# Optimization experiments

Hardware: AMD Instinct MI355X
Metric: run time of the kernel (lower is better)

The kernel has to match this reference:

```python
import jax, jax.numpy as jnp
import numpy as np
from jax import lax

LEAK = 0.2
EPS = 1e-5
T = 20  # sequence_length


def _lrelu(x):
    return jnp.where(x >= 0, x, LEAK * x)


def _deconv(x, w, stride=2, k=4, p=1):
    # PyTorch ConvTranspose2d(weight [in,out,kH,kW], stride=2, pad=1) equivalent:
    # flip kernel spatially, swap in/out channels, use lhs_dilation.
    wt = jnp.flip(w, (2, 3)).transpose(1, 0, 2, 3)  # OIHW
    pad = k - 1 - p
    return lax.conv_general_dilated(
        x, wt, window_strides=(1, 1), padding=[(pad, pad), (pad, pad)],
        lhs_dilation=(stride, stride),
        dimension_numbers=('NCHW', 'OIHW', 'NCHW'))


def _bn(x, g, b):
    # BatchNorm2d, training mode (batch statistics, biased variance)
    m = x.mean((0, 2, 3), keepdims=True)
    v = x.var((0, 2, 3), keepdims=True)
    return (x - m) * lax.rsqrt(v + EPS) * g[None, :, None, None] + b[None, :, None, None]


def setup_inputs() -> dict:
    B, CD, MD, H, FF = 64, 128, 128, 256, 512
    ks = jax.random.split(jax.random.key(0), 32)
    rn = lambda k, sh, s=0.02: (s * jax.random.normal(k, sh)).astype(jnp.float32)
    return {
        'z_content': jax.random.normal(ks[0], (B, CD), jnp.float32),
        'z_motion': jax.random.normal(ks[1], (B, MD), jnp.float32),
        'W_h': rn(ks[2], (H, CD + MD)), 'b_h': jnp.zeros((H,), jnp.float32),
        'W_c': rn(ks[3], (H, CD + MD)), 'b_c': jnp.zeros((H,), jnp.float32),
        'W_ih': rn(ks[4], (4 * H, H)), 'W_hh': rn(ks[5], (4 * H, H)),
        'b_ih': jnp.zeros((4 * H,), jnp.float32), 'b_hh': jnp.zeros((4 * H,), jnp.float32),
        'W_f': rn(ks[6], (FF, H)), 'b_f': jnp.zeros((FF,), jnp.float32),
        'init_in': rn(ks[7], (1, H), 0.1),
        'fc_W': rn(ks[8], (256 * 4 * 4, FF + CD)), 'fc_b': jnp.zeros((256 * 16,), jnp.float32),
        'w0': rn(ks[9], (256, 128, 4, 4)), 'g0': jnp.ones((128,), jnp.float32), 'be0': jnp.zeros((128,), jnp.float32),
        'w1': rn(ks[10], (128, 64, 4, 4)), 'g1': jnp.ones((64,), jnp.float32), 'be1': jnp.zeros((64,), jnp.float32),
        'w2': rn(ks[11], (64, 32, 4, 4)), 'g2': jnp.ones((32,), jnp.float32), 'be2': jnp.zeros((32,), jnp.float32),
        'wf': rn(ks[12], (32, 1, 4, 4)), 'bf': jnp.zeros((1,), jnp.float32),
    }


def reference(z_content, z_motion, W_h, b_h, W_c, b_c, W_ih, W_hh, b_ih, b_hh,
              W_f, b_f, init_in, fc_W, fc_b, w0, g0, be0, w1, g1, be1,
              w2, g2, be2, wf, bf):
    B = z_content.shape[0]
    z = jnp.concatenate([z_content, z_motion], axis=-1)
    h0 = z @ W_h.T + b_h  # [B,H]
    c0 = z @ W_c.T + b_c
    x0 = jnp.broadcast_to(init_in, (B, init_in.shape[1]))
    bias = b_ih + b_hh

    def step(carry, _):
        x, h, c = carry
        gates = x @ W_ih.T + h @ W_hh.T + bias  # [B,4H], torch gate order i,f,g,o
        i, f, g, o = jnp.split(gates, 4, axis=-1)
        c_new = jax.nn.sigmoid(f) * c + jax.nn.sigmoid(i) * jnp.tanh(g)
        h_new = jax.nn.sigmoid(o) * jnp.tanh(c_new)
        return (h_new, h_new, c_new), h_new

    _, outs = lax.scan(step, (x0, h0, c0), None, length=T)  # [T,B,H]
    outs = outs.transpose(1, 0, 2)  # [B,T,H]

    ff = _lrelu(outs @ W_f.T + b_f)  # [B,T,FF]
    zc = jnp.broadcast_to(z_content[:, None, :], (B, T, z_content.shape[1]))
    feat = jnp.concatenate([ff, zc], axis=-1).reshape(B * T, -1)  # [B*T, FF+CD]

    h = _lrelu(feat @ fc_W.T + fc_b).reshape(B * T, 256, 4, 4)
    h = _lrelu(_bn(_deconv(h, w0), g0, be0))   # [B*T,128,8,8]
    h = _lrelu(_bn(_deconv(h, w1), g1, be1))   # [B*T,64,16,16]
    h = _lrelu(_bn(_deconv(h, w2), g2, be2))   # [B*T,32,32,32]
    out = jax.nn.sigmoid(_deconv(h, wf) + bf[None, :, None, None])  # [B*T,1,64,64]
    return out.reshape(B, T, *out.shape[1:])
```

## Files before the change

kernel.cpp:

```cpp
#include <hip/hip_runtime.h>
#include <hip/hip_bf16.h>
#include <math.h>

typedef __hip_bfloat16 bf16;
typedef __attribute__((ext_vector_type(8))) short bf16x8;
typedef __attribute__((ext_vector_type(4))) float f32x4;
typedef __attribute__((ext_vector_type(2))) float f32x2;

#define LRELU(v) ((v) > 0.f ? (v) : 0.2f*(v))

__device__ __forceinline__ float sig_f(float x){ return 1.f/(1.f + __expf(-x)); }
__device__ __forceinline__ float tanh_f(float x){
  float ax = fabsf(x);
  float e = __expf(-2.f*ax);
  float t = (1.f - e)/(1.f + e);
  return x >= 0.f ? t : -t;
}
__device__ __forceinline__ ushort bfbits(float v){
  bf16 b = __float2bfloat16(v);
  return *(ushort*)&b;
}
__device__ __forceinline__ uint bfpack(float a, float b){
  return (uint)bfbits(a) | ((uint)bfbits(b) << 16);
}
__device__ __forceinline__ float bflo(uint u){ return __uint_as_float(u << 16); }
__device__ __forceinline__ float bfhi(uint u){ return __uint_as_float(u & 0xffff0000u); }

__global__ void k_tobf16(const float* __restrict__ src, ushort* __restrict__ dst, int n){
  int i = blockIdx.x*256 + threadIdx.x;
  if (i < n) dst[i] = bfbits(src[i]);
}

__global__ void k_transpose(const float* __restrict__ src, float* __restrict__ dst, int R, int C){
  __shared__ float t[32][33];
  int c0 = blockIdx.x*32, r0 = blockIdx.y*32;
  int tx = threadIdx.x, ty = threadIdx.y;
  #pragma unroll
  for (int i = 0; i < 4; ++i)
    t[ty+8*i][tx] = src[(size_t)(r0+ty+8*i)*C + c0+tx];
  __syncthreads();
  #pragma unroll
  for (int i = 0; i < 4; ++i)
    dst[(size_t)(c0+ty+8*i)*R + r0+tx] = t[tx][ty+8*i];
}

__global__ void k_w4prep(const float* __restrict__ Wih, const float* __restrict__ Whh,
                         uint4* __restrict__ Whq8, uint4* __restrict__ Wsq8,
                         float* __restrict__ stats){
  int k4 = blockIdx.x, j = threadIdx.x;
  if (k4 < 2) { int i = k4*256 + j; if (i < 448) stats[i] = 0.f; }
  uint h4[4], s4[4];
  #pragma unroll
  for (int d = 0; d < 4; ++d) {
    int k = 4*k4 + d;
    float hi = Whh[j*256+k],       hf = Whh[(256+j)*256+k];
    float hg = Whh[(512+j)*256+k], ho = Whh[(768+j)*256+k];
    float ii = Wih[j*256+k],       iff = Wih[(256+j)*256+k];
    float ig = Wih[(512+j)*256+k], io = Wih[(768+j)*256+k];
    int lo = __builtin_amdgcn_cvt_pk_fp8_f32(hi, hf, 0, false);
    h4[d] = (uint)__builtin_amdgcn_cvt_pk_fp8_f32(hg, ho, lo, true);
    lo = __builtin_amdgcn_cvt_pk_fp8_f32(hi+ii, hf+iff, 0, false);
    s4[d] = (uint)__builtin_amdgcn_cvt_pk_fp8_f32(hg+ig, ho+io, lo, true);
  }
  Whq8[k4*256+j] = make_uint4(h4[0], h4[1], h4[2], h4[3]);
  Wsq8[k4*256+j] = make_uint4(s4[0], s4[1], s4[2], s4[3]);
}

__global__ void k_xgbias(const float* __restrict__ Wih, const float* __restrict__ b_ih,
                         const float* __restrict__ b_hh, const float* __restrict__ init_in,
                         float4* __restrict__ xg4, float4* __restrict__ bias4){
  int b = blockIdx.x, t = threadIdx.x;
  float v = init_in[t];
  float p0 = v * Wih[b*256 + t];
  float p1 = v * Wih[(256+b)*256 + t];
  float p2 = v * Wih[(512+b)*256 + t];
  float p3 = v * Wih[(768+b)*256 + t];
  #pragma unroll
  for (int o = 32; o; o >>= 1) {
    p0 += __shfl_xor(p0, o); p1 += __shfl_xor(p1, o);
    p2 += __shfl_xor(p2, o); p3 += __shfl_xor(p3, o);
  }
  __shared__ float4 red[4];
  int lane = t & 63, wid = t >> 6;
  if (lane == 0) red[wid] = make_float4(p0,p1,p2,p3);
  __syncthreads();
  if (t == 0) {
    float4 bi = make_float4(b_ih[b]+b_hh[b], b_ih[256+b]+b_hh[256+b],
                            b_ih[512+b]+b_hh[512+b], b_ih[768+b]+b_hh[768+b]);
    bias4[b] = bi;
    float4 a = bi;
    #pragma unroll
    for (int w = 0; w < 4; ++w) { a.x += red[w].x; a.y += red[w].y; a.z += red[w].z; a.w += red[w].w; }
    xg4[b] = a;
  }
}

__global__ __launch_bounds__(256) void k_h0c0(const float* __restrict__ zc, const float* __restrict__ zm,
                      const float* __restrict__ WhT, const float* __restrict__ WcT,
                      const float* __restrict__ b_h, const float* __restrict__ b_c,
                      float* __restrict__ h, float* __restrict__ c){
  __shared__ float zs[256];
  int b = blockIdx.x, j = threadIdx.x;
  zs[j] = (j < 128) ? zc[b*128 + j] : zm[b*128 + (j-128)];
  __syncthreads();
  float ah = b_h[j], ac = b_c[j];
  #pragma unroll 4
  for (int k = 0; k < 256; ++k) {
    float zv = zs[k];
    ah = fmaf(zv, WhT[k*256 + j], ah);
    ac = fmaf(zv, WcT[k*256 + j], ac);
  }
  h[b*256+j] = ah; c[b*256+j] = ac;
}

__global__ __launch_bounds__(1024) void k_lstm_all(
    const uint4* __restrict__ Whq8, const uint4* __restrict__ Wsq8,
    const float4* __restrict__ xg4, const float4* __restrict__ bias4,
    const float* __restrict__ h0, const float* __restrict__ c0,
    ushort* __restrict__ outsb){
  __shared__ float hs[256];
  __shared__ float4 part[3][256];
  const int b = blockIdx.x, tid = threadIdx.x;
  const int j = tid & 255, kq = tid >> 8;
  float cj = 0.f;
  if (kq == 0) { hs[j] = h0[b*256 + j]; cj = c0[b*256 + j]; }
  __syncthreads();
  for (int t = 0; t < 20; ++t) {
    const uint4* __restrict__ Wp = ((t == 0) ? Whq8 : Wsq8) + (size_t)(kq*16)*256 + j;
    float4 a = make_float4(0.f, 0.f, 0.f, 0.f);
    #pragma unroll 8
    for (int kk = 0; kk < 16; ++kk) {
      uint4 wv = Wp[(size_t)kk*256];
      const float* __restrict__ hb = &hs[kq*64 + 4*kk];
      {
        f32x2 pif = __builtin_amdgcn_cvt_pk_f32_fp8((int)wv.x, false);
        f32x2 pgo = __builtin_amdgcn_cvt_pk_f32_fp8((int)wv.x, true);
        float hv = hb[0];
        a.x = fmaf(hv, pif[0], a.x); a.y = fmaf(hv, pif[1], a.y);
        a.z = fmaf(hv, pgo[0], a.z); a.w = fmaf(hv, pgo[1], a.w);
      }
      {
        f32x2 pif = __builtin_amdgcn_cvt_pk_f32_fp8((int)wv.y, false);
        f32x2 pgo = __builtin_amdgcn_cvt_pk_f32_fp8((int)wv.y, true);
        float hv = hb[1];
        a.x = fmaf(hv, pif[0], a.x); a.y = fmaf(hv, pif[1], a.y);
        a.z = fmaf(hv, pgo[0], a.z); a.w = fmaf(hv, pgo[1], a.w);
      }
      {
        f32x2 pif = __builtin_amdgcn_cvt_pk_f32_fp8((int)wv.z, false);
        f32x2 pgo = __builtin_amdgcn_cvt_pk_f32_fp8((int)wv.z, true);
        float hv = hb[2];
        a.x = fmaf(hv, pif[0], a.x); a.y = fmaf(hv, pif[1], a.y);
        a.z = fmaf(hv, pgo[0], a.z); a.w = fmaf(hv, pgo[1], a.w);
      }
      {
        f32x2 pif = __builtin_amdgcn_cvt_pk_f32_fp8((int)wv.w, false);
        f32x2 pgo = __builtin_amdgcn_cvt_pk_f32_fp8((int)wv.w, true);
        float hv = hb[3];
        a.x = fmaf(hv, pif[0], a.x); a.y = fmaf(hv, pif[1], a.y);
        a.z = fmaf(hv, pgo[0], a.z); a.w = fmaf(hv, pgo[1], a.w);
      }
    }
    if (kq) part[kq-1][j] = a;
    __syncthreads();
    if (kq == 0) {
      float4 p1 = part[0][j], p2 = part[1][j], p3 = part[2][j];
      float4 bb = (t == 0) ? xg4[j] : bias4[j];
      a.x += p1.x + p2.x + p3.x + bb.x;
      a.y += p1.y + p2.y + p3.y + bb.y;
      a.z += p1.z + p2.z + p3.z + bb.z;
      a.w += p1.w + p2.w + p3.w + bb.w;
      float ig = sig_f(a.x), fg = sig_f(a.y), gg = tanh_f(a.z), og = sig_f(a.w);
      cj = fmaf(fg, cj, ig*gg);
      float hj = og * tanh_f(cj);
      outsb[(b*20 + t)*256 + j] = bfbits(hj);
      hs[j] = hj;
    }
    __syncthreads();
  }
}

__global__ void k_zc(const float* __restrict__ zc, ushort* __restrict__ featb){
  int e = blockIdx.x*256 + threadIdx.x;
  int r = e >> 7, c = e & 127;
  featb[r*640 + 512 + c] = bfbits(zc[(r/20)*128 + c]);
}

__global__ __launch_bounds__(256) void k_ff_m(
    const ushort* __restrict__ A, const ushort* __restrict__ W,
    const float* __restrict__ bias, ushort* __restrict__ C)
{
  constexpr int K = 256, BK = 64, NK = K/BK, BM = 128, BN = 64;
  constexpr int RS = 72;
  constexpr int NCF = BN/16;
  constexpr int AC = 4, WC = 2;

  __shared__ __align__(16) ushort Al[2][BM*RS];
  __shared__ __align__(16) ushort Wl[2][BN*RS];

  const int tid = threadIdx.x;
  const int col0 = blockIdx.x * BN, row0 = blockIdx.y * BM;
  const int w = tid >> 6, l = tid & 63, lm = l & 15, lk = l >> 4;

  f32x4 acc[NCF][2];
  #pragma unroll
  for (int m = 0; m < NCF; ++m)
    #pragma unroll
    for (int s = 0; s < 2; ++s)
      acc[m][s] = (f32x4){0.f,0.f,0.f,0.f};

  uint4 ar[AC], wr[WC];

  #define LOADG(kt) { \
    _Pragma("unroll") \
    for (int i = 0; i < AC; ++i) { \
      int chunk = tid + i*256; \
      int rl = chunk >> 3, kc = chunk & 7; \
      ar[i] = *(const uint4*)&A[(size_t)(row0+rl)*K + (kt)*BK + kc*8]; \
    } \
    _Pragma("unroll") \
    for (int i = 0; i < WC; ++i) { \
      int chunk = tid + i*256; \
      int co = chunk >> 3, kc = chunk & 7; \
      wr[i] = *(const uint4*)&W[(size_t)(col0+co)*K + (kt)*BK + kc*8]; \
    } }

  #define STOREL(buf) { \
    _Pragma("unroll") \
    for (int i = 0; i < AC; ++i) { \
      int chunk = tid + i*256; \
      int rl = chunk >> 3, kc = chunk & 7; \
      *(uint4*)&Al[buf][rl*RS + kc*8] = ar[i]; \
    } \
    _Pragma("unroll") \
    for (int i = 0; i < WC; ++i) { \
      int chunk = tid + i*256; \
      int co = chunk >> 3, kc = chunk & 7; \
      *(uint4*)&Wl[buf][co*RS + kc*8] = wr[i]; \
    } }

  LOADG(0);
  STOREL(0);
  int cur = 0;
  for (int kt = 0; kt < NK; ++kt) {
    if (kt + 1 < NK) LOADG(kt + 1);
    __syncthreads();
    #pragma unroll
    for (int kf = 0; kf < 2; ++kf) {
      bf16x8 bfr[2];
      #pragma unroll
      for (int s = 0; s < 2; ++s)
        bfr[s] = *(bf16x8*)&Al[cur][(w*32 + s*16 + lm)*RS + kf*32 + lk*8];
      #pragma unroll
      for (int m = 0; m < NCF; ++m) {
        bf16x8 afr = *(bf16x8*)&Wl[cur][(m*16 + lm)*RS + kf*32 + lk*8];
        acc[m][0] = __builtin_amdgcn_mfma_f32_16x16x32_bf16(afr, bfr[0], acc[m][0], 0, 0, 0);
        acc[m][1] = __builtin_amdgcn_mfma_f32_16x16x32_bf16(afr, bfr[1], acc[m][1], 0, 0, 0);
      }
    }
    if (kt + 1 < NK) STOREL(cur ^ 1);
    cur ^= 1;
  }

  #pragma unroll
  for (int m = 0; m < NCF; ++m) {
    #pragma unroll
    for (int s = 0; s < 2; ++s) {
      int row = row0 + w*32 + s*16 + lm;
      f32x4 v = acc[m][s];
      int u0 = col0 + m*16 + lk*4;
      union { ushort u[4]; uint2 q; } pk;
      #pragma unroll
      for (int j = 0; j < 4; ++j)
        pk.u[j] = bfbits(LRELU(v[j] + bias[u0+j]));
      *(uint2*)&C[(size_t)row*640 + u0] = pk.q;
    }
  }
  #undef LOADG
  #undef STOREL
}

__global__ __launch_bounds__(256) void k_gemm_fc_m(
    const ushort* __restrict__ A, const ushort* __restrict__ W,
    const float* __restrict__ bias, ushort* __restrict__ C)
{
  constexpr int K = 640, BK = 64, NK = K/BK, BM = 128, BN = 64;
  constexpr int RS = 72;
  constexpr int NCF = BN/16;
  constexpr int AC = 4, WC = 2;

  __shared__ __align__(16) ushort Al[2][BM*RS];
  __shared__ __align__(16) ushort Wl[2][BN*RS];

  const int tid = threadIdx.x;
  const int col0 = blockIdx.x * BN, row0 = blockIdx.y * BM;
  const int w = tid >> 6, l = tid & 63, lm = l & 15, lk = l >> 4;

  f32x4 acc[NCF][2];
  #pragma unroll
  for (int m = 0; m < NCF; ++m)
    #pragma unroll
    for (int s = 0; s < 2; ++s)
      acc[m][s] = (f32x4){0.f,0.f,0.f,0.f};

  uint4 ar[AC], wr[WC];

  #define LOADG(kt) { \
    _Pragma("unroll") \
    for (int i = 0; i < AC; ++i) { \
      int chunk = tid + i*256; \
      int rl = chunk >> 3, kc = chunk & 7; \
      ar[i] = *(const uint4*)&A[(size_t)(row0+rl)*K + (kt)*BK + kc*8]; \
    } \
    _Pragma("unroll") \
    for (int i = 0; i < WC; ++i) { \
      int chunk = tid + i*256; \
      int co = chunk >> 3, kc = chunk & 7; \
      wr[i] = *(const uint4*)&W[(size_t)(col0+co)*K + (kt)*BK + kc*8]; \
    } }

  #define STOREL(buf) { \
    _Pragma("unroll") \
    for (int i = 0; i < AC; ++i) { \
      int chunk = tid + i*256; \
      int rl = chunk >> 3, kc = chunk & 7; \
      *(uint4*)&Al[buf][rl*RS + kc*8] = ar[i]; \
    } \
    _Pragma("unroll") \
    for (int i = 0; i < WC; ++i) { \
      int chunk = tid + i*256; \
      int co = chunk >> 3, kc = chunk & 7; \
      *(uint4*)&Wl[buf][co*RS + kc*8] = wr[i]; \
    } }

  LOADG(0);
  STOREL(0);
  int cur = 0;
  for (int kt = 0; kt < NK; ++kt) {
    if (kt + 1 < NK) LOADG(kt + 1);
    __syncthreads();
    #pragma unroll
    for (int kf = 0; kf < 2; ++kf) {
      bf16x8 bfr[2];
      #pragma unroll
      for (int s = 0; s < 2; ++s)
        bfr[s] = *(bf16x8*)&Al[cur][(w*32 + s*16 + lm)*RS + kf*32 + lk*8];
      #pragma unroll
      for (int m = 0; m < NCF; ++m) {
        bf16x8 afr = *(bf16x8*)&Wl[cur][(m*16 + lm)*RS + kf*32 + lk*8];
        acc[m][0] = __builtin_amdgcn_mfma_f32_16x16x32_bf16(afr, bfr[0], acc[m][0], 0, 0, 0);
        acc[m][1] = __builtin_amdgcn_mfma_f32_16x16x32_bf16(afr, bfr[1], acc[m][1], 0, 0, 0);
      }
    }
    if (kt + 1 < NK) STOREL(cur ^ 1);
    cur ^= 1;
  }

  #pragma unroll
  for (int m = 0; m < NCF; ++m) {
    #pragma unroll
    for (int s = 0; s < 2; ++s) {
      int row = row0 + w*32 + s*16 + lm;
      f32x4 v = acc[m][s];
      #pragma unroll
      for (int j = 0; j < 4; ++j) {
        int u = col0 + m*16 + lk*4 + j;
        float val = LRELU(v[j] + bias[u]);
        C[((size_t)row << 12) + ((size_t)(u & 15) << 8) + (u >> 4)] = bfbits(val);
      }
    }
  }
  #undef LOADG
  #undef STOREL
}

template<int CI, int CO>
__global__ void k_wprep_im(const float* __restrict__ w, ushort* __restrict__ wpn){
  constexpr int K = 4*CI, KF = K/32, MMW2 = CO/16;
  int e = blockIdx.x*256 + threadIdx.x;
  if (e >= 16*CI*CO) return;
  int j  = e & 7;
  int lk = (e >> 3) & 3;
  int lm = (e >> 5) & 15;
  int r3 = e >> 9;
  int kf = r3 % KF; int r4 = r3 / KF;
  int m  = r4 % MMW2; int p = r4 / MMW2;
  int k  = kf*32 + lk*8 + j;
  int t  = k / CI, ci = k % CI;
  int co = m*16 + lm;
  int py = p >> 1, px = p & 1, dy = t >> 1, dx = t & 1;
  int ky = (py ? 0 : 1) + 2*dy;
  int kx = (px ? 0 : 1) + 2*dx;
  wpn[e] = bfbits(w[((ci*CO + co)*4 + ky)*4 + kx]);
}

__global__ void k_wfprep(const float* __restrict__ wf, ushort* __restrict__ wfb){
  int e = blockIdx.x*256 + threadIdx.x;
  if (e < 512) {
    int t = e >> 5, ci = e & 31;
    wfb[t*32 + ci] = bfbits(wf[ci*16 + t]);
  }
}

template<int CI, int CO, int HI>
__global__ __launch_bounds__(256) void k_dcv(
    const ushort* __restrict__ in, const ushort* __restrict__ wp,
    ushort* __restrict__ out, float* __restrict__ gsum, float* __restrict__ gsq)
{
  constexpr int WI = HI, HO = 2*HI, WO = 2*WI;
  constexpr int K = 4*CI, BK = 64, NK = K/BK, KFT = K/32;
  constexpr int BSP = 128;
  constexpr int RS = 72;
  constexpr int NCF = CO/16;
  constexpr int AC = BSP/32;

  __shared__ __align__(16) ushort Al[2][BSP*RS];
  __shared__ float s_sum[CO], s_sq[CO];

  const int tid = threadIdx.x;
  const int sp0 = blockIdx.x * BSP;
  const int p  = blockIdx.y;
  const int py = p >> 1, px = p & 1;
  const int w  = tid >> 6, l = tid & 63;
  const int lm = l & 15, lk = l >> 4;

  if (tid < CO) { s_sum[tid] = 0.f; s_sq[tid] = 0.f; }

  f32x4 acc[NCF][2];
  #pragma unroll
  for (int m = 0; m < NCF; ++m)
    #pragma unroll
    for (int s = 0; s < 2; ++s)
      acc[m][s] = (f32x4){0.f,0.f,0.f,0.f};

  uint4 ar[AC];
  const ushort* wpb = wp + (size_t)(p*NCF)*KFT*512;

  #define LOADT(kt) { \
    int t = ((kt)*BK)/CI, ci0 = ((kt)*BK)%CI; \
    int dy = t >> 1, dx = t & 1; \
    _Pragma("unroll") \
    for (int i = 0; i < AC; ++i) { \
      int chunk = tid + i*256; \
      int rl = chunk >> 3, kc = chunk & 7; \
      int r = sp0 + rl; \
      int n = r / (HI*WI), rem = r % (HI*WI); \
      int oy = rem / WI, ox = rem % WI; \
      int iy = oy + py - dy, ix = ox + px - dx; \
      if ((unsigned)iy < (unsigned)HI && (unsigned)ix < (unsigned)WI) \
        ar[i] = *(const uint4*)&in[((((size_t)n*HI + iy)*WI + ix)*CI) + ci0 + kc*8]; \
      else ar[i] = make_uint4(0,0,0,0); \
    } }

  #define STORET(buf) { \
    _Pragma("unroll") \
    for (int i = 0; i < AC; ++i) { \
      int chunk = tid + i*256; \
      int rl = chunk >> 3, kc = chunk & 7; \
      *(uint4*)&Al[buf][rl*RS + kc*8] = ar[i]; \
    } }

  LOADT(0);
  STORET(0);
  int cur = 0;
  for (int kt = 0; kt < NK; ++kt) {
    if (kt + 1 < NK) LOADT(kt + 1);
    __syncthreads();
    #pragma unroll
    for (int kf = 0; kf < 2; ++kf) {
      const int ktg = kt*2 + kf;
      bf16x8 bfr[2];
      #pragma unroll
      for (int s = 0; s < 2; ++s)
        bfr[s] = *(bf16x8*)&Al[cur][(w*32 + s*16 + lm)*RS + kf*32 + lk*8];
      #pragma unroll
      for (int m = 0; m < NCF; ++m) {
        bf16x8 afr = *(const bf16x8*)&wpb[((size_t)m*KFT + ktg)*512 + lm*32 + lk*8];
        acc[m][0] = __builtin_amdgcn_mfma_f32_16x16x32_bf16(afr, bfr[0], acc[m][0], 0, 0, 0);
        acc[m][1] = __builtin_amdgcn_mfma_f32_16x16x32_bf16(afr, bfr[1], acc[m][1], 0, 0, 0);
      }
    }
    if (kt + 1 < NK) STORET(cur ^ 1);
    cur ^= 1;
  }

  #pragma unroll
  for (int m = 0; m < NCF; ++m) {
    float s1[4] = {0,0,0,0}, s2[4] = {0,0,0,0};
    #pragma unroll
    for (int s = 0; s < 2; ++s) {
      f32x4 v = acc[m][s];
      #pragma unroll
      for (int j = 0; j < 4; ++j) { s1[j] += v[j]; s2[j] += v[j]*v[j]; }
    }
    #pragma unroll
    for (int j = 0; j < 4; ++j) {
      float a = s1[j], b = s2[j];
      #pragma unroll
      for (int o = 1; o < 16; o <<= 1) { a += __shfl_xor(a, o); b += __shfl_xor(b, o); }
      if (lm == 0) {
        atomicAdd(&s_sum[m*16 + lk*4 + j], a);
        atomicAdd(&s_sq [m*16 + lk*4 + j], b);
      }
    }
  }
  #pragma unroll
  for (int s = 0; s < 2; ++s) {
    int sp = sp0 + w*32 + s*16 + lm;
    int n = sp / (HI*WI), rem = sp % (HI*WI);
    int y = 2*(rem / WI) + py, x = 2*(rem % WI) + px;
    size_t ob = (((size_t)n*HO + y)*WO + x)*CO + lk*4;
    #pragma unroll
    for (int m = 0; m < NCF; ++m) {
      f32x4 v = acc[m][s];
      union { ushort u[4]; uint2 q; } pk;
      pk.u[0] = bfbits(v[0]); pk.u[1] = bfbits(v[1]);
      pk.u[2] = bfbits(v[2]); pk.u[3] = bfbits(v[3]);
      *(uint2*)&out[ob + m*16] = pk.q;
    }
  }
  __syncthreads();
  for (int cc = tid; cc < CO; cc += 256) {
    atomicAdd(&gsum[cc], s_sum[cc]);
    atomicAdd(&gsq[cc],  s_sq[cc]);
  }
  #undef LOADT
  #undef STORET
}

template<int CI, int CO, int HI>
__global__ __launch_bounds__(512) void k_dcvim(
    const ushort* __restrict__ in, const ushort* __restrict__ wp,
    const float* __restrict__ gsumP, const float* __restrict__ gsqP,
    const float* __restrict__ gP, const float* __restrict__ beP, float invNP,
    ushort* __restrict__ out, float* __restrict__ gsum, float* __restrict__ gsq)
{
  constexpr int WI = HI, HO = 2*HI, WO = 2*WI;
  constexpr int K = 4*CI;
  constexpr int KF = K/32;
  constexpr int PAD = HI + 2;
  constexpr int CICH = CI/8;
  constexpr int MMW2 = CO/16;
  constexpr int SFTH = HI*WI/32;

  __shared__ __align__(16) ushort Ain[PAD*PAD*CI];
  __shared__ float s_sum[CO], s_sq[CO];
  __shared__ float s_scale[CI], s_shift[CI];

  const int tid = threadIdx.x;
  const int n = blockIdx.x;
  const int w = tid >> 6, l = tid & 63, lm = l & 15, lk = l >> 4;
  const int p = w >> 1, py = p >> 1, px = p & 1, ph = w & 1;

  if (tid < CO) { s_sum[tid] = 0.f; s_sq[tid] = 0.f; }
  if (tid >= 512-CI) {
    int c = tid - (512-CI);
    float m = gsumP[c]*invNP;
    float v = gsqP[c]*invNP - m*m;
    float sc = gP[c]*rsqrtf(v + 1e-5f);
    s_scale[c] = sc;
    s_shift[c] = beP[c] - m*sc;
  }
  __syncthreads();

  const ushort* inb = in + (size_t)n * HI * WI * CI;
  constexpr int NPCH = PAD*PAD*CICH;
  for (int e = tid; e < NPCH; e += 512) {
    int ci8 = e % CICH; int sp = e / CICH;
    int c = sp % PAD, r = sp / PAD;
    int chS = ci8 ^ (c & 7);
    if (r >= 1 && r <= HI && c >= 1 && c <= WI) {
      uint4 u = *(const uint4*)&inb[(((size_t)(r-1)*WI + (c-1))*CI) + ci8*8];
      int ci0 = ci8*8;
      float4 sc0 = *(const float4*)&s_scale[ci0];
      float4 sc1 = *(const float4*)&s_scale[ci0+4];
      float4 sh0 = *(const float4*)&s_shift[ci0];
      float4 sh1 = *(const float4*)&s_shift[ci0+4];
      float v0 = LRELU(fmaf(bflo(u.x), sc0.x, sh0.x));
      float v1 = LRELU(fmaf(bfhi(u.x), sc0.y, sh0.y));
      float v2 = LRELU(fmaf(bflo(u.y), sc0.z, sh0.z));
      float v3 = LRELU(fmaf(bfhi(u.y), sc0.w, sh0.w));
      float v4 = LRELU(fmaf(bflo(u.z), sc1.x, sh1.x));
      float v5 = LRELU(fmaf(bfhi(u.z), sc1.y, sh1.y));
      float v6 = LRELU(fmaf(bflo(u.w), sc1.z, sh1.z));
      float v7 = LRELU(fmaf(bfhi(u.w), sc1.w, sh1.w));
      uint4 o;
      o.x = (uint)bfpack(v0, v1);
      o.y = (uint)bfpack(v2, v3);
      o.z = (uint)bfpack(v4, v5);
      o.w = (uint)bfpack(v6, v7);
      ((uint4*)Ain)[(r*PAD + c)*CICH + chS] = o;
    } else {
      ((uint4*)Ain)[(r*PAD + c)*CICH + chS] = make_uint4(0,0,0,0);
    }
  }
  __syncthreads();

  f32x4 acc[MMW2][SFTH];
  #pragma unroll
  for (int m = 0; m < MMW2; ++m)
    #pragma unroll
    for (int sf = 0; sf < SFTH; ++sf)
      acc[m][sf] = (f32x4){0.f,0.f,0.f,0.f};

  const ushort* wpb = wp + (size_t)(p*MMW2)*KF*512;
  #pragma unroll
  for (int kf = 0; kf < KF; ++kf) {
    const int t = (kf*32)/CI, cib = (kf*32)%CI;
    const int dy = t >> 1, dx = t & 1;
    bf16x8 afr[MMW2];
    #pragma unroll
    for (int m = 0; m < MMW2; ++m)
      afr[m] = *(const bf16x8*)&wpb[((size_t)m*KF + kf)*512 + lm*32 + lk*8];
    const int ch = (cib >> 3) + lk;
    #pragma unroll
    for (int sf = 0; sf < SFTH; ++sf) {
      int s = (ph*SFTH + sf)*16 + lm;
      int y = s / WI, x = s % WI;
      int r = y + py - dy + 1, c = x + px - dx + 1;
      bf16x8 bfr = *(const bf16x8*)&Ain[((r*PAD + c)*CICH + (ch ^ (c & 7)))*8];
      #pragma unroll
      for (int m = 0; m < MMW2; ++m)
        acc[m][sf] = __builtin_amdgcn_mfma_f32_16x16x32_bf16(afr[m], bfr, acc[m][sf], 0, 0, 0);
    }
  }

  float s1[MMW2][4], s2[MMW2][4];
  #pragma unroll
  for (int m = 0; m < MMW2; ++m)
    #pragma unroll
    for (int j = 0; j < 4; ++j) { s1[m][j] = 0.f; s2[m][j] = 0.f; }

  #pragma unroll
  for (int sf = 0; sf < SFTH; ++sf) {
    int s = (ph*SFTH + sf)*16 + lm;
    int y = 2*(s / WI) + py, x = 2*(s % WI) + px;
    size_t ob = (((size_t)n*HO + y)*WO + x)*CO + lk*4;
    #pragma unroll
    for (int m = 0; m < MMW2; ++m) {
      f32x4 v = acc[m][sf];
      union { ushort u[4]; uint2 q; } pk;
      #pragma unroll
      for (int j = 0; j < 4; ++j) {
        pk.u[j] = bfbits(v[j]);
        s1[m][j] += v[j];
        s2[m][j] += v[j]*v[j];
      }
      *(uint2*)&out[ob + m*16] = pk.q;
    }
  }

  #pragma unroll
  for (int m = 0; m < MMW2; ++m) {
    #pragma unroll
    for (int j = 0; j < 4; ++j) {
      float a = s1[m][j], b = s2[m][j];
      #pragma unroll
      for (int o = 1; o < 16; o <<= 1) { a += __shfl_xor(a, o); b += __shfl_xor(b, o); }
      if (lm == 0) {
        atomicAdd(&s_sum[m*16 + lk*4 + j], a);
        atomicAdd(&s_sq [m*16 + lk*4 + j], b);
      }
    }
  }

  __syncthreads();
  for (int cc = tid; cc < CO; cc += 512) {
    atomicAdd(&gsum[cc], s_sum[cc]);
    atomicAdd(&gsq[cc],  s_sq[cc]);
  }
}

__global__ __launch_bounds__(256) void k_final(
    const ushort* __restrict__ in, const ushort* __restrict__ wfb,
    const float* __restrict__ gsumP, const float* __restrict__ gsqP,
    const float* __restrict__ gP, const float* __restrict__ beP, float invNP,
    const float* __restrict__ bfb, float* __restrict__ outp)
{
  constexpr int CI=32, HI=32, WI=32, HO=64, WO=64, SPLIT=4, HOq=HO/SPLIT;
  constexpr int RMAX = 10;
  constexpr int DP = 20;
  __shared__ float Dl[RMAX*32*DP];
  __shared__ float s_scale[CI], s_shift[CI];

  const int tid = threadIdx.x, bid = blockIdx.x;
  const int n = bid % 1280, q = bid / 1280;
  const int y0 = q * HOq;
  const int rows_lo = max(0, y0/2 - 1);
  const int rows_hi = min(HI-1, (y0 + HOq)/2);
  const int nrows = rows_hi - rows_lo + 1;

  if (tid < CI) {
    float m = gsumP[tid]*invNP;
    float v = gsqP[tid]*invNP - m*m;
    float sc = gP[tid]*rsqrtf(v + 1e-5f);
    s_scale[tid] = sc;
    s_shift[tid] = beP[tid] - m*sc;
  }
  __syncthreads();

  const int w = tid >> 6, l = tid & 63, lm = l & 15, lk = l >> 4;
  const bf16x8 afr = *(const bf16x8*)&wfb[lm*32 + lk*8];
  const float4 sc0 = *(const float4*)&s_scale[lk*8];
  const float4 sc1 = *(const float4*)&s_scale[lk*8+4];
  const float4 sh0 = *(const float4*)&s_shift[lk*8];
  const float4 sh1 = *(const float4*)&s_shift[lk*8+4];

  const ushort* inb = in + (size_t)n * HI * WI * CI;
  const int ngrp = nrows * 2;
  for (int g = w; g < ngrp; g += 4) {
    int px = g*16 + lm;
    int rl = px >> 5, ix = px & 31;
    uint4 u = *(const uint4*)&inb[(((size_t)(rows_lo+rl)*WI + ix)*CI) + lk*8];
    float v0 = LRELU(fmaf(bflo(u.x), sc0.x, sh0.x));
    float v1 = LRELU(fmaf(bfhi(u.x), sc0.y, sh0.y));
    float v2 = LRELU(fmaf(bflo(u.y), sc0.z, sh0.z));
    float v3 = LRELU(fmaf(bfhi(u.y), sc0.w, sh0.w));
    float v4 = LRELU(fmaf(bflo(u.z), sc1.x, sh1.x));
    float v5 = LRELU(fmaf(bfhi(u.z), sc1.y, sh1.y));
    float v6 = LRELU(fmaf(bflo(u.w), sc1.z, sh1.z));
    float v7 = LRELU(fmaf(bfhi(u.w), sc1.w, sh1.w));
    union { uint uu[4]; bf16x8 v; } pk;
    pk.uu[0] = bfpack(v0, v1);
    pk.uu[1] = bfpack(v2, v3);
    pk.uu[2] = bfpack(v4, v5);
    pk.uu[3] = bfpack(v6, v7);
    f32x4 d = __builtin_amdgcn_mfma_f32_16x16x32_bf16(afr, pk.v, (f32x4){0.f,0.f,0.f,0.f}, 0, 0, 0);
    *(f32x4*)&Dl[px*DP + lk*4] = d;
  }
  __syncthreads();

  const float b0 = bfb[0];
  #pragma unroll
  for (int i = 0; i < (HOq*WO)/256; ++i) {
    int e = tid + i*256;
    int oy = e >> 6, x = e & 63;
    int y = y0 + oy;
    int kya = (y + 1) & 1, iya = (y + 1) >> 1;
    int kxa = (x + 1) & 1, ixa = (x + 1) >> 1;
    float acc = b0;
    #pragma unroll
    for (int dy = 0; dy < 2; ++dy) {
      int iy = iya - dy, ky = kya + 2*dy;
      if (iy < 0 || iy >= HI) continue;
      #pragma unroll
      for (int dx = 0; dx < 2; ++dx) {
        int ix = ixa - dx, kx = kxa + 2*dx;
        if (ix < 0 || ix >= WI) continue;
        acc += Dl[((iy - rows_lo)*WI + ix)*DP + (ky*4 + kx)];
      }
    }
    outp[(size_t)n*HO*WO + y*WO + x] = 1.f/(1.f + __expf(-acc));
  }
}

extern "C" void kernel_launch(void* const* d_in, const int* in_sizes, int n_in,
                              void* d_out, int out_size, void* d_ws, size_t ws_size,
                              hipStream_t stream) {
  const float* z_content = (const float*)d_in[0];
  const float* z_motion  = (const float*)d_in[1];
  const float* W_h  = (const float*)d_in[2];
  const float* b_h  = (const float*)d_in[3];
  const float* W_c  = (const float*)d_in[4];
  const float* b_c  = (const float*)d_in[5];
  const float* W_ih = (const float*)d_in[6];
  const float* W_hh = (const float*)d_in[7];
  const float* b_ih = (const float*)d_in[8];
  const float* b_hh = (const float*)d_in[9];
  const float* W_f  = (const float*)d_in[10];
  const float* b_f  = (const float*)d_in[11];
  const float* init_in = (const float*)d_in[12];
  const float* fc_W = (const float*)d_in[13];
  const float* fc_b = (const float*)d_in[14];
  const float* w0 = (const float*)d_in[15];
  const float* g0 = (const float*)d_in[16];
  const float* be0 = (const float*)d_in[17];
  const float* w1 = (const float*)d_in[18];
  const float* g1 = (const float*)d_in[19];
  const float* be1 = (const float*)d_in[20];
  const float* w2 = (const float*)d_in[21];
  const float* g2 = (const float*)d_in[22];
  const float* be2 = (const float*)d_in[23];
  const float* wf = (const float*)d_in[24];
  const float* bf_ = (const float*)d_in[25];

  const size_t P_BYTES = 10631168;
  const size_t X_OFF   = P_BYTES;
  const size_t X_BYTES = 83886080;
  const size_t Y_OFF   = X_OFF + X_BYTES;
  const size_t NEED    = Y_OFF + 41943040;
  if (ws_size < NEED) return;

  float* ws = (float*)d_ws;
  char*  wsb = (char*)d_ws;
  float* sum0 = ws + 0;        float* sq0 = ws + 128;
  float* sum1 = ws + 256;      float* sq1 = ws + 320;
  float* sum2 = ws + 384;      float* sq2 = ws + 416;
  float4* xg4   = (float4*)(ws + 1024);
  float4* bias4 = (float4*)(ws + 2048);
  float* h    = ws + 3072;
  float* c    = ws + 19456;
  ushort* outsb = (ushort*)(ws + 35840);
  float* WhT  = ws + 199680;
  float* WcT  = ws + 265216;
  uint4* Whq8 = (uint4*)(ws + 330752);
  uint4* Wsq8 = (uint4*)(ws + 592896);
  ushort* wp0 = (ushort*)(ws + 855040);
  ushort* wp1 = (ushort*)(ws + 1117184);
  ushort* wp2 = (ushort*)(ws + 1182720);
  ushort* wfb = (ushort*)(ws + 1199104);
  ushort* wpff = (ushort*)(ws + 1199616);
  ushort* featb = (ushort*)(ws + 1265152);

  ushort* wpfc = (ushort*)(wsb + X_OFF);
  ushort* out0 = (ushort*)(wsb + X_OFF);
  ushort* out2 = (ushort*)(wsb + X_OFF);
  ushort* h1   = (ushort*)(wsb + Y_OFF);
  ushort* out1 = (ushort*)(wsb + Y_OFF);

  dim3 tb(32,8);
  k_transpose<<<dim3(8,8),   tb, 0, stream>>>(W_h,  WhT, 256, 256);
  k_transpose<<<dim3(8,8),   tb, 0, stream>>>(W_c,  WcT, 256, 256);
  k_tobf16<<<10240, 256, 0, stream>>>(fc_W, wpfc, 2621440);
  k_tobf16<<<512, 256, 0, stream>>>(W_f, wpff, 131072);
  k_w4prep<<<64, 256, 0, stream>>>(W_ih, W_hh, Whq8, Wsq8, ws);
  k_xgbias<<<256, 256, 0, stream>>>(W_ih, b_ih, b_hh, init_in, xg4, bias4);
  k_h0c0<<<64, 256, 0, stream>>>(z_content, z_motion, WhT, WcT, b_h, b_c, h, c);
  k_wprep_im<256,128><<<2048, 256, 0, stream>>>(w0, wp0);
  k_wprep_im<128,64><<<512, 256, 0, stream>>>(w1, wp1);
  k_wprep_im<64,32><<<128, 256, 0, stream>>>(w2, wp2);
  k_wfprep<<<2, 256, 0, stream>>>(wf, wfb);

  k_lstm_all<<<64, 1024, 0, stream>>>(Whq8, Wsq8, xg4, bias4, h, c, outsb);

  k_ff_m<<<dim3(8, 10), 256, 0, stream>>>(outsb, wpff, b_f, featb);
  k_zc<<<640, 256, 0, stream>>>(z_content, featb);
  k_gemm_fc_m<<<dim3(64, 10), 256, 0, stream>>>(featb, wpfc, fc_b, h1);

  k_dcv<256,128,4><<<dim3(160,4), 256, 0, stream>>>(h1, wp0, out0, sum0, sq0);
  k_dcvim<128,64,8><<<1280, 512, 0, stream>>>(out0, wp1, sum0, sq0, g0, be0, 1.f/81920.f, out1, sum1, sq1);
  k_dcvim<64,32,16><<<1280, 512, 0, stream>>>(out1, wp2, sum1, sq1, g1, be1, 1.f/327680.f, out2, sum2, sq2);
  k_final<<<5120, 256, 0, stream>>>(out2, wfb, sum2, sq2, g2, be2, 1.f/1310720.f, bf_, (float*)d_out);
}
```

Before: 453.2 us.

## Specialize first deconv to load whole 4x4 inputs into LDS once

Replaces the generic double-buffered im2col deconv kernel for the first layer with a specialized kernel. Each block now loads four full 4x4x256 input images into swizzled shared memory once, and builds the im2col fragments from LDS per k-step, zero-filling out-of-bounds taps. The per-k-tile global gathers and the double-buffer syncs go away. Each wave now covers 16 output pixels instead of 32, and the grid doubles. This halves weight-fragment reuse per block and raises global weight reads.

```diff
diff --git a/kernel.cpp b/kernel.cpp
--- a/kernel.cpp
+++ b/kernel.cpp
@@ -402,100 +402,87 @@
   }
 }
 
-template<int CI, int CO, int HI>
-__global__ __launch_bounds__(256) void k_dcv(
+__global__ __launch_bounds__(256) void k_dcv0(
     const ushort* __restrict__ in, const ushort* __restrict__ wp,
     ushort* __restrict__ out, float* __restrict__ gsum, float* __restrict__ gsq)
 {
-  constexpr int WI = HI, HO = 2*HI, WO = 2*WI;
-  constexpr int K = 4*CI, BK = 64, NK = K/BK, KFT = K/32;
-  constexpr int BSP = 128;
-  constexpr int RS = 72;
-  constexpr int NCF = CO/16;
-  constexpr int AC = BSP/32;
-
-  __shared__ __align__(16) ushort Al[2][BSP*RS];
+  constexpr int CI = 256, CO = 128, HO = 8, WO = 8;
+  constexpr int KF = 32, MMW = 8;
+  constexpr int CICH = CI/8;
+
+  __shared__ __align__(16) ushort Ain[4*16*CI];
   __shared__ float s_sum[CO], s_sq[CO];
 
   const int tid = threadIdx.x;
-  const int sp0 = blockIdx.x * BSP;
-  const int p  = blockIdx.y;
-  const int py = p >> 1, px = p & 1;
-  const int w  = tid >> 6, l = tid & 63;
-  const int lm = l & 15, lk = l >> 4;
+  const int n0 = blockIdx.x * 4;
+  const int p = blockIdx.y, py = p >> 1, pxp = p & 1;
+  const int w = tid >> 6, l = tid & 63, lm = l & 15, lk = l >> 4;
 
   if (tid < CO) { s_sum[tid] = 0.f; s_sq[tid] = 0.f; }
 
-  f32x4 acc[NCF][2];
-  #pragma unroll
-  for (int m = 0; m < NCF; ++m)
-    #pragma unroll
-    for (int s = 0; s < 2; ++s)
-      acc[m][s] = (f32x4){0.f,0.f,0.f,0.f};
-
-  uint4 ar[AC];
-  const ushort* wpb = wp + (size_t)(p*NCF)*KFT*512;
-
-  #define LOADT(kt) { \
-    int t = ((kt)*BK)/CI, ci0 = ((kt)*BK)%CI; \
-    int dy = t >> 1, dx = t & 1; \
-    _Pragma("unroll") \
-    for (int i = 0; i < AC; ++i) { \
-      int chunk = tid + i*256; \
-      int rl = chunk >> 3, kc = chunk & 7; \
-      int r = sp0 + rl; \
-      int n = r / (HI*WI), rem = r % (HI*WI); \
-      int oy = rem / WI, ox = rem % WI; \
-      int iy = oy + py - dy, ix = ox + px - dx; \
-      if ((unsigned)iy < (unsigned)HI && (unsigned)ix < (unsigned)WI) \
-        ar[i] = *(const uint4*)&in[((((size_t)n*HI + iy)*WI + ix)*CI) + ci0 + kc*8]; \
-      else ar[i] = make_uint4(0,0,0,0); \
-    } }
-
-  #define STORET(buf) { \
-    _Pragma("unroll") \
-    for (int i = 0; i < AC; ++i) { \
-      int chunk = tid + i*256; \
-      int rl = chunk >> 3, kc = chunk & 7; \
-      *(uint4*)&Al[buf][rl*RS + kc*8] = ar[i]; \
-    } }
-
-  LOADT(0);
-  STORET(0);
-  int cur = 0;
-  for (int kt = 0; kt < NK; ++kt) {
-    if (kt + 1 < NK) LOADT(kt + 1);
-    __syncthreads();
-    #pragma unroll
-    for (int kf = 0; kf < 2; ++kf) {
-      const int ktg = kt*2 + kf;
-      bf16x8 bfr[2];
-      #pragma unroll
-      for (int s = 0; s < 2; ++s)
-        bfr[s] = *(bf16x8*)&Al[cur][(w*32 + s*16 + lm)*RS + kf*32 + lk*8];
-      #pragma unroll
-      for (int m = 0; m < NCF; ++m) {
-        bf16x8 afr = *(const bf16x8*)&wpb[((size_t)m*KFT + ktg)*512 + lm*32 + lk*8];
-        acc[m][0] = __builtin_amdgcn_mfma_f32_16x16x32_bf16(afr, bfr[0], acc[m][0], 0, 0, 0);
-        acc[m][1] = __builtin_amdgcn_mfma_f32_16x16x32_bf16(afr, bfr[1], acc[m][1], 0, 0, 0);
-      }
-    }
-    if (kt + 1 < NK) STORET(cur ^ 1);
-    cur ^= 1;
-  }
-
-  #pragma unroll
-  for (int m = 0; m < NCF; ++m) {
-    float s1[4] = {0,0,0,0}, s2[4] = {0,0,0,0};
-    #pragma unroll
-    for (int s = 0; s < 2; ++s) {
-      f32x4 v = acc[m][s];
-      #pragma unroll
-      for (int j = 0; j < 4; ++j) { s1[j] += v[j]; s2[j] += v[j]*v[j]; }
-    }
+  const ushort* inb = in + (size_t)n0 * 16 * CI;
+  #pragma unroll
+  for (int i = 0; i < 8; ++i) {
+    int e = tid + i*256;
+    int ci8 = e & 31; int sp = e >> 5;
+    uint4 u = *(const uint4*)&inb[(size_t)sp*CI + ci8*8];
+    int px = sp & 15;
+    ((uint4*)Ain)[sp*CICH + (ci8 ^ (px & 7))] = u;
+  }
+  __syncthreads();
+
+  f32x4 acc[MMW];
+  #pragma unroll
+  for (int m = 0; m < MMW; ++m) acc[m] = (f32x4){0.f,0.f,0.f,0.f};
+
+  const int oy = lm >> 2, ox = lm & 3;
+  const ushort* wpb = wp + (size_t)(p*MMW)*KF*512;
+  #pragma unroll
+  for (int kf = 0; kf < KF; ++kf) {
+    const int t = kf >> 3;
+    const int dy = t >> 1, dx = t & 1;
+    const int ch = ((kf & 7) << 2) + lk;
+    int iy = oy + py - dy, ix = ox + pxp - dx;
+    bool valid = ((unsigned)iy < 4u) && ((unsigned)ix < 4u);
+    int pix = iy*4 + ix;
+    bf16x8 bfr = (bf16x8){0,0,0,0,0,0,0,0};
+    if (valid)
+      bfr = *(const bf16x8*)&Ain[((w*16 + pix)*CICH + (ch ^ (pix & 7)))*8];
+    #pragma unroll
+    for (int m = 0; m < MMW; ++m) {
+      bf16x8 afr = *(const bf16x8*)&wpb[((size_t)m*KF + kf)*512 + lm*32 + lk*8];
+      acc[m] = __builtin_amdgcn_mfma_f32_16x16x32_bf16(afr, bfr, acc[m], 0, 0, 0);
+    }
+  }
+
+  float s1[MMW][4], s2[MMW][4];
+  #pragma unroll
+  for (int m = 0; m < MMW; ++m)
     #pragma unroll
     for (int j = 0; j < 4; ++j) {
-      float a = s1[j], b = s2[j];
+      float v = acc[m][j];
+      s1[m][j] = v; s2[m][j] = v*v;
+    }
+
+  {
+    int n = n0 + w;
+    int y = 2*oy + py, x = 2*ox + pxp;
+    size_t ob = (((size_t)n*HO + y)*WO + x)*CO + lk*4;
+    #pragma unroll
+    for (int m = 0; m < MMW; ++m) {
+      f32x4 v = acc[m];
+      union { ushort u[4]; uint2 q; } pk;
+      pk.u[0] = bfbits(v[0]); pk.u[1] = bfbits(v[1]);
+      pk.u[2] = bfbits(v[2]); pk.u[3] = bfbits(v[3]);
+      *(uint2*)&out[ob + m*16] = pk.q;
+    }
+  }
+
+  #pragma unroll
+  for (int m = 0; m < MMW; ++m) {
+    #pragma unroll
+    for (int j = 0; j < 4; ++j) {
+      float a = s1[m][j], b = s2[m][j];
       #pragma unroll
       for (int o = 1; o < 16; o <<= 1) { a += __shfl_xor(a, o); b += __shfl_xor(b, o); }
       if (lm == 0) {
@@ -504,28 +491,11 @@
       }
     }
   }
-  #pragma unroll
-  for (int s = 0; s < 2; ++s) {
-    int sp = sp0 + w*32 + s*16 + lm;
-    int n = sp / (HI*WI), rem = sp % (HI*WI);
-    int y = 2*(rem / WI) + py, x = 2*(rem % WI) + px;
-    size_t ob = (((size_t)n*HO + y)*WO + x)*CO + lk*4;
-    #pragma unroll
-    for (int m = 0; m < NCF; ++m) {
-      f32x4 v = acc[m][s];
-      union { ushort u[4]; uint2 q; } pk;
-      pk.u[0] = bfbits(v[0]); pk.u[1] = bfbits(v[1]);
-      pk.u[2] = bfbits(v[2]); pk.u[3] = bfbits(v[3]);
-      *(uint2*)&out[ob + m*16] = pk.q;
-    }
-  }
   __syncthreads();
   for (int cc = tid; cc < CO; cc += 256) {
     atomicAdd(&gsum[cc], s_sum[cc]);
     atomicAdd(&gsq[cc],  s_sq[cc]);
   }
-  #undef LOADT
-  #undef STORET
 }
 
 template<int CI, int CO, int HI>
@@ -837,7 +807,7 @@
   k_zc<<<640, 256, 0, stream>>>(z_content, featb);
   k_gemm_fc_m<<<dim3(64, 10), 256, 0, stream>>>(featb, wpfc, fc_b, h1);
 
-  k_dcv<256,128,4><<<dim3(160,4), 256, 0, stream>>>(h1, wp0, out0, sum0, sq0);
+  k_dcv0<<<dim3(320, 4), 256, 0, stream>>>(h1, wp0, out0, sum0, sq0);
   k_dcvim<128,64,8><<<1280, 512, 0, stream>>>(out0, wp1, sum0, sq0, g0, be0, 1.f/81920.f, out1, sum1, sq1);
   k_dcvim<64,32,16><<<1280, 512, 0, stream>>>(out1, wp2, sum1, sq1, g1, be1, 1.f/327680.f, out2, sum2, sq2);
   k_final<<<5120, 256, 0, stream>>>(out2, wfb, sum2, sq2, g2, be2, 1.f/1310720.f, bf_, (float*)d_out);
```

After: 480.5 us. 1.06x slower.
